# Kernel tuning notes

Hardware: AMD Instinct MI355X
Metric: run time of the kernel (lower is better)

The kernel has to match this reference:

```python
import jax, jax.numpy as jnp
import numpy as np

# HOG config (matches init_kwargs / skimage defaults for block_norm='L2-Hys')
ORIENTATIONS = 9
CELL = 8          # pixels_per_cell (square)
BLOCK = 2         # cells_per_block (square)
EPS = 1e-5        # skimage block-norm epsilon


def setup_inputs() -> dict:
    key = jax.random.key(0)
    x = jax.random.uniform(key, (64, 1, 512, 512), dtype=jnp.float32)
    return {"x": x}


def _hog(img):
    # img: (B, H, W) grayscale float
    B, H, W = img.shape
    # skimage _hog_channel_gradient: central differences, zero at borders
    g_row = jnp.zeros_like(img).at[:, 1:-1, :].set(img[:, 2:, :] - img[:, :-2, :])
    g_col = jnp.zeros_like(img).at[:, :, 1:-1].set(img[:, :, 2:] - img[:, :, :-2])
    mag = jnp.hypot(g_row, g_col)
    # unsigned orientation in [0, 180)
    ori = jnp.degrees(jnp.arctan2(g_row, g_col)) % 180.0
    bin_width = 180.0 / ORIENTATIONS
    bin_idx = jnp.minimum((ori / bin_width).astype(jnp.int32), ORIENTATIONS - 1)

    ncr, ncc = H // CELL, W // CELL  # number of cells per row/col
    mag_c = mag[:, : ncr * CELL, : ncc * CELL].reshape(B, ncr, CELL, ncc, CELL)
    bin_c = bin_idx[:, : ncr * CELL, : ncc * CELL].reshape(B, ncr, CELL, ncc, CELL)

    # per-cell orientation histogram; skimage averages by cell area
    hists = []
    for i in range(ORIENTATIONS):  # small fixed loop over 9 bins
        hists.append(jnp.where(bin_c == i, mag_c, 0.0).sum(axis=(2, 4)))
    hist = jnp.stack(hists, axis=-1) / (CELL * CELL)  # (B, ncr, ncc, O)

    # sliding blocks of BLOCK x BLOCK cells, stride 1 cell
    nbr, nbc = ncr - BLOCK + 1, ncc - BLOCK + 1
    tmp = jnp.stack([hist[:, br : br + nbr] for br in range(BLOCK)], axis=2)       # (B,nbr,BLOCK,ncc,O)
    blocks = jnp.stack([tmp[:, :, :, bc : bc + nbc] for bc in range(BLOCK)], axis=4)  # (B,nbr,BLOCK,nbc,BLOCK,O)
    blocks = blocks.transpose(0, 1, 3, 2, 4, 5)  # (B, nbr, nbc, BLOCK, BLOCK, O)

    # L2-Hys normalization (skimage default block_norm)
    n1 = jnp.sqrt(jnp.sum(blocks * blocks, axis=(-3, -2, -1), keepdims=True) + EPS**2)
    b = jnp.minimum(blocks / n1, 0.2)
    n2 = jnp.sqrt(jnp.sum(b * b, axis=(-3, -2, -1), keepdims=True) + EPS**2)
    normalized = b / n2
    return normalized.reshape(B, -1)  # feature_vector=True ravel per image


def reference(x):
    return _hog(x[:, 0, :, :].astype(jnp.float32))
```

## Files before the change

kernel.cpp:

```cpp
#include <hip/hip_runtime.h>


#define ORIENT 9
#define CELLPX 8
#define IMH 512
#define IMW 512
#define NCR 64
#define NCC 64
#define NBR 63
#define NBC 63
#define NIMG 64

__global__ __launch_bounds__(512) void hog_cell_hist(const float* __restrict__ img,
                                                     float* __restrict__ hist) {
    __shared__ float lhist[CELLPX * ORIENT];
    const int tx = threadIdx.x;
    const int ty = threadIdx.y;
    const int tid = ty * 64 + tx;

    if (tid < CELLPX * ORIENT) lhist[tid] = 0.0f;
    __syncthreads();

    const int c = blockIdx.x * 64 + tx;
    const int r = blockIdx.y * 8 + ty;
    const int b = blockIdx.z;
    const float* im = img + (size_t)b * IMH * IMW;

    float gr = 0.0f, gc = 0.0f;
    if (r > 0 && r < IMH - 1)
        gr = im[(size_t)(r + 1) * IMW + c] - im[(size_t)(r - 1) * IMW + c];
    if (c > 0 && c < IMW - 1)
        gc = im[(size_t)r * IMW + c + 1] - im[(size_t)r * IMW + c - 1];

    float mag = sqrtf(gr * gr + gc * gc);
    float ori = atan2f(gr, gc) * 57.29577951308232f;
    ori = fmodf(ori, 180.0f);
    if (ori < 0.0f) ori += 180.0f;
    int bin = (int)(ori / 20.0f);
    bin = bin > (ORIENT - 1) ? (ORIENT - 1) : bin;

    atomicAdd(&lhist[(tx >> 3) * ORIENT + bin], mag);
    __syncthreads();

    if (tid < CELLPX * ORIENT) {
        const int cell = tid / ORIENT;
        const int o    = tid % ORIENT;
        const int cellRow = blockIdx.y;
        const int cellCol = blockIdx.x * 8 + cell;
        hist[(((size_t)b * NCR + cellRow) * NCC + cellCol) * ORIENT + o] =
            lhist[tid] * (1.0f / 64.0f);
    }
}

__global__ __launch_bounds__(256) void hog_block_norm(const float* __restrict__ hist,
                                                      float* __restrict__ out) {
    const int total = NIMG * NBR * NBC;
    int t = blockIdx.x * blockDim.x + threadIdx.x;
    if (t >= total) return;

    const int bc = t % NBC;
    const int br = (t / NBC) % NBR;
    const int b  = t / (NBC * NBR);

    float v[36];
    float s = 0.0f;
#pragma unroll
    for (int i = 0; i < 2; ++i) {
        const float* row = hist + (((size_t)b * NCR + br + i) * NCC + bc) * ORIENT;
#pragma unroll
        for (int k = 0; k < 18; ++k) {
            float h = row[k];
            v[i * 18 + k] = h;
            s += h * h;
        }
    }
    const float n1 = sqrtf(s + 1e-10f);
    float s2 = 0.0f;
#pragma unroll
    for (int k = 0; k < 36; ++k) {
        float x = fminf(v[k] / n1, 0.2f);
        v[k] = x;
        s2 += x * x;
    }
    const float n2 = sqrtf(s2 + 1e-10f);

    float* o = out + (size_t)t * 36;
#pragma unroll
    for (int k = 0; k < 36; ++k) o[k] = v[k] / n2;
}

extern "C" void kernel_launch(void* const* d_in, const int* in_sizes, int n_in,
                              void* d_out, int out_size, void* d_ws, size_t ws_size,
                              hipStream_t stream) {
    const float* x  = (const float*)d_in[0];
    float* out      = (float*)d_out;
    float* hist     = (float*)d_ws;

    dim3 b1(64, 8, 1);
    dim3 g1(IMW / 64, IMH / 8, NIMG);
    hipLaunchKernelGGL(hog_cell_hist, g1, b1, 0, stream, x, hist);

    const int total = NIMG * NBR * NBC;
    dim3 b2(256, 1, 1);
    dim3 g2((total + 255) / 256, 1, 1);
    hipLaunchKernelGGL(hog_block_norm, g2, b2, 0, stream, hist, out);
}
```

Before: 218.5 us.

## Process eight pixels per thread with vectorized loads and private cell histograms

Result: faster. 188.4 us (-13.8%).

```diff
diff --git a/kernel.cpp b/kernel.cpp
--- a/kernel.cpp
+++ b/kernel.cpp
@@ -2,7 +2,6 @@
 
 
 #define ORIENT 9
-#define CELLPX 8
 #define IMH 512
 #define IMW 512
 #define NCR 64
@@ -11,45 +10,54 @@
 #define NBC 63
 #define NIMG 64
 
-__global__ __launch_bounds__(512) void hog_cell_hist(const float* __restrict__ img,
+__global__ __launch_bounds__(256) void hog_cell_hist(const float* __restrict__ img,
                                                      float* __restrict__ hist) {
-    __shared__ float lhist[CELLPX * ORIENT];
+    __shared__ float lh[32 * ORIENT];
     const int tx = threadIdx.x;
     const int ty = threadIdx.y;
-    const int tid = ty * 64 + tx;
+    const int tid = ty * 32 + tx;
 
-    if (tid < CELLPX * ORIENT) lhist[tid] = 0.0f;
+    lh[tid] = 0.f;
+    if (tid < 32) lh[tid + 256] = 0.f;
     __syncthreads();
 
-    const int c = blockIdx.x * 64 + tx;
-    const int r = blockIdx.y * 8 + ty;
-    const int b = blockIdx.z;
-    const float* im = img + (size_t)b * IMH * IMW;
+    const int c0 = blockIdx.x * 256 + tx * 8;
+    const int r  = blockIdx.y * 8 + ty;
+    const float* im = img + (size_t)blockIdx.z * (IMH * IMW) + (size_t)r * IMW + c0;
 
-    float gr = 0.0f, gc = 0.0f;
-    if (r > 0 && r < IMH - 1)
-        gr = im[(size_t)(r + 1) * IMW + c] - im[(size_t)(r - 1) * IMW + c];
-    if (c > 0 && c < IMW - 1)
-        gc = im[(size_t)r * IMW + c + 1] - im[(size_t)r * IMW + c - 1];
+    const float4* imv = (const float4*)im;
+    float4 a0 = imv[0], b0 = imv[1];
+    float4 am = {0,0,0,0}, bm = {0,0,0,0};
+    float4 ap = {0,0,0,0}, bp = {0,0,0,0};
+    const bool rin = (r > 0) && (r < IMH - 1);
+    if (r > 0)       { const float4* p = (const float4*)(im - IMW); am = p[0]; bm = p[1]; }
+    if (r < IMH - 1) { const float4* p = (const float4*)(im + IMW); ap = p[0]; bp = p[1]; }
+    const float left  = (c0 > 0)       ? im[-1] : 0.f;
+    const float right = (c0 + 8 < IMW) ? im[8]  : 0.f;
 
-    float mag = sqrtf(gr * gr + gc * gc);
-    float ori = atan2f(gr, gc) * 57.29577951308232f;
-    ori = fmodf(ori, 180.0f);
-    if (ori < 0.0f) ori += 180.0f;
-    int bin = (int)(ori / 20.0f);
-    bin = bin > (ORIENT - 1) ? (ORIENT - 1) : bin;
+    float rv[10] = {left, a0.x, a0.y, a0.z, a0.w, b0.x, b0.y, b0.z, b0.w, right};
+    float pv[8]  = {ap.x, ap.y, ap.z, ap.w, bp.x, bp.y, bp.z, bp.w};
+    float mv[8]  = {am.x, am.y, am.z, am.w, bm.x, bm.y, bm.z, bm.w};
 
-    atomicAdd(&lhist[(tx >> 3) * ORIENT + bin], mag);
+    float* cellh = &lh[tx * ORIENT];
+#pragma unroll
+    for (int j = 0; j < 8; ++j) {
+        const float gr = rin ? (pv[j] - mv[j]) : 0.f;
+        const bool cin = (c0 + j > 0) && (c0 + j < IMW - 1);
+        const float gc = cin ? (rv[j + 2] - rv[j]) : 0.f;
+        const float mag = sqrtf(gr * gr + gc * gc);
+        float ori = atan2f(gr, gc) * 57.29577951308232f;
+        ori = (ori >= 180.0f) ? ori - 180.0f : ori;
+        ori = (ori <   0.0f) ? ori + 180.0f : ori;
+        int bin = (int)(ori / 20.0f);
+        bin = bin > (ORIENT - 1) ? (ORIENT - 1) : bin;
+        atomicAdd(&cellh[bin], mag);
+    }
     __syncthreads();
 
-    if (tid < CELLPX * ORIENT) {
-        const int cell = tid / ORIENT;
-        const int o    = tid % ORIENT;
-        const int cellRow = blockIdx.y;
-        const int cellCol = blockIdx.x * 8 + cell;
-        hist[(((size_t)b * NCR + cellRow) * NCC + cellCol) * ORIENT + o] =
-            lhist[tid] * (1.0f / 64.0f);
-    }
+    float* hrow = hist + (((size_t)blockIdx.z * NCR + blockIdx.y) * NCC + blockIdx.x * 32) * ORIENT;
+    hrow[tid] = lh[tid] * (1.f / 64.f);
+    if (tid < 32) hrow[tid + 256] = lh[tid + 256] * (1.f / 64.f);
 }
 
 __global__ __launch_bounds__(256) void hog_block_norm(const float* __restrict__ hist,
@@ -63,41 +71,38 @@
     const int b  = t / (NBC * NBR);
 
     float v[36];
-    float s = 0.0f;
+    float s = 0.f;
 #pragma unroll
     for (int i = 0; i < 2; ++i) {
         const float* row = hist + (((size_t)b * NCR + br + i) * NCC + bc) * ORIENT;
 #pragma unroll
-        for (int k = 0; k < 18; ++k) {
-            float h = row[k];
-            v[i * 18 + k] = h;
-            s += h * h;
-        }
+        for (int k = 0; k < 18; ++k) { float h = row[k]; v[i * 18 + k] = h; s += h * h; }
     }
-    const float n1 = sqrtf(s + 1e-10f);
-    float s2 = 0.0f;
+    const float r1 = 1.0f / sqrtf(s + 1e-10f);
+    float s2 = 0.f;
 #pragma unroll
     for (int k = 0; k < 36; ++k) {
-        float x = fminf(v[k] / n1, 0.2f);
+        float x = fminf(v[k] * r1, 0.2f);
         v[k] = x;
         s2 += x * x;
     }
-    const float n2 = sqrtf(s2 + 1e-10f);
+    const float r2 = 1.0f / sqrtf(s2 + 1e-10f);
 
-    float* o = out + (size_t)t * 36;
+    float4* o = (float4*)(out + (size_t)t * 36);
 #pragma unroll
-    for (int k = 0; k < 36; ++k) o[k] = v[k] / n2;
+    for (int k = 0; k < 9; ++k)
+        o[k] = make_float4(v[4*k] * r2, v[4*k+1] * r2, v[4*k+2] * r2, v[4*k+3] * r2);
 }
 
 extern "C" void kernel_launch(void* const* d_in, const int* in_sizes, int n_in,
                               void* d_out, int out_size, void* d_ws, size_t ws_size,
                               hipStream_t stream) {
-    const float* x  = (const float*)d_in[0];
-    float* out      = (float*)d_out;
-    float* hist     = (float*)d_ws;
+    const float* x = (const float*)d_in[0];
+    float* out  = (float*)d_out;
+    float* hist = (float*)d_ws;
 
-    dim3 b1(64, 8, 1);
-    dim3 g1(IMW / 64, IMH / 8, NIMG);
+    dim3 b1(32, 8, 1);
+    dim3 g1(IMW / 256, IMH / 8, NIMG);
     hipLaunchKernelGGL(hog_cell_hist, g1, b1, 0, stream, x, hist);
 
     const int total = NIMG * NBR * NBC;
```
